# Optimization experiments

Measured on AMD Instinct MI355X. Metric: run time of the kernel, lower is better.

The kernel has to match this reference:

```python
import jax, jax.numpy as jnp
import numpy as np

B, C, H, W = 4, 128, 96, 96
E = 4
C8 = C // 8


def _conv1x1(w, b, x):
    # w: [out, in], x: [b, in, H, W]
    return jnp.einsum('oi,bihw->bohw', w, x) + b[None, :, None, None]


def _bilinear_zeros(x, gx, gy):
    # x: [b, C, h, w]; gx, gy: [b, H2, W2] normalized coords in [-1, 1]
    # align_corners=True, padding_mode='zeros' (matches F.grid_sample)
    b, c, h, w = x.shape
    ix = (gx + 1.0) * 0.5 * (w - 1)
    iy = (gy + 1.0) * 0.5 * (h - 1)
    ix0 = jnp.floor(ix)
    iy0 = jnp.floor(iy)
    tx = ix - ix0
    ty = iy - iy0
    ix0 = ix0.astype(jnp.int32)
    iy0 = iy0.astype(jnp.int32)

    def gather(yy, xx):
        valid = ((xx >= 0) & (xx < w) & (yy >= 0) & (yy < h)).astype(x.dtype)
        xc = jnp.clip(xx, 0, w - 1)
        yc = jnp.clip(yy, 0, h - 1)
        vals = jax.vmap(lambda xb, y, xi: xb[:, y, xi])(x, yc, xc)  # [b,C,H2,W2]
        return vals * valid[:, None]

    w00 = ((1 - tx) * (1 - ty))[:, None]
    w01 = (tx * (1 - ty))[:, None]
    w10 = ((1 - tx) * ty)[:, None]
    w11 = (tx * ty)[:, None]
    return (gather(iy0, ix0) * w00 + gather(iy0, ix0 + 1) * w01
            + gather(iy0 + 1, ix0) * w10 + gather(iy0 + 1, ix0 + 1) * w11)


def setup_inputs() -> dict:
    key = jax.random.key(0)
    ks = jax.random.split(key, 12)
    s = 0.05
    return {
        'x': jax.random.normal(ks[0], (B, C, H, W), jnp.float32),
        'weight_compress': jax.random.normal(ks[1], (E, C8, C), jnp.float32) * s,
        'weight_expand': jax.random.normal(ks[2], (E, C, C8), jnp.float32) * s,
        'body_w1': jax.random.normal(ks[3], (64, 3), jnp.float32) * s,
        'body_b1': jax.random.normal(ks[4], (64,), jnp.float32) * s,
        'body_w2': jax.random.normal(ks[5], (64, 64), jnp.float32) * s,
        'body_b2': jax.random.normal(ks[6], (64,), jnp.float32) * s,
        'rout_w': jax.random.normal(ks[7], (E, 64), jnp.float32) * s,
        'rout_b': jax.random.normal(ks[8], (E,), jnp.float32) * s,
        'off_w': jax.random.normal(ks[9], (2, 64), jnp.float32) * s,
        'off_b': jax.random.normal(ks[10], (2,), jnp.float32) * s,
        'scale': 2,
    }


def reference(x, weight_compress, weight_expand, body_w1, body_b1,
              body_w2, body_b2, rout_w, rout_b, off_w, off_b, scale):
    b, c, h, w = x.shape
    sc = float(scale)
    H2 = round(h * sc)
    W2 = round(w * sc)

    # fractional sub-pixel coordinates (meta-upsample positional encoding)
    ch = (jnp.arange(H2, dtype=jnp.float32) + 0.5) / sc
    ch = ch - jnp.floor(ch + 0.001) - 0.5  # [H2]
    cw = (jnp.arange(W2, dtype=jnp.float32) + 0.5) / sc
    cw = cw - jnp.floor(cw + 0.001) - 0.5  # [W2]
    inp = jnp.stack([
        jnp.full((H2, W2), 1.0 / sc, jnp.float32),
        jnp.broadcast_to(ch[:, None], (H2, W2)),
        jnp.broadcast_to(cw[None, :], (H2, W2)),
    ], axis=0)[None]  # [1, 3, H2, W2]

    emb = jax.nn.relu(_conv1x1(body_w1, body_b1, inp))
    emb = jax.nn.relu(_conv1x1(body_w2, body_b2, emb))
    offset = _conv1x1(off_w, off_b, emb)                      # [1, 2, H2, W2]
    routing = jax.nn.sigmoid(_conv1x1(rout_w, rout_b, emb))   # [1, E, H2, W2]
    r = routing[0].transpose(1, 2, 0)                         # [H2, W2, E]

    # base sampling grid, align_corners=True normalization + learned offset
    gx = ((jnp.arange(W2, dtype=jnp.float32) + 0.5) / sc - 0.5) * 2.0 / (w - 1) - 1.0
    gy = ((jnp.arange(H2, dtype=jnp.float32) + 0.5) / sc - 0.5) * 2.0 / (h - 1) - 1.0
    gx = gx[None, None, :] + offset[:, 0] * 2.0 / (w - 1)     # [1, H2, W2]
    gy = gy[None, :, None] + offset[:, 1] * 2.0 / (h - 1)
    gx = jnp.broadcast_to(gx, (b, H2, W2))
    gy = jnp.broadcast_to(gy, (b, H2, W2))

    fea0 = _bilinear_zeros(x, gx, gy)          # [b, C, H2, W2]
    fea = fea0.transpose(0, 2, 3, 1)           # [b, H2, W2, C]

    # per-pixel routed 1x1 convs: compress (C->C/8) then expand (C/8->C)
    comp = jnp.einsum('bhwc,hwe,eoc->bhwo', fea, r, weight_compress)
    out = jnp.einsum('bhwo,hwe,eco->bhwc', comp, r, weight_expand)
    return out.transpose(0, 3, 1, 2) + fea0
```

## Files before the change

### kernel.cpp

```cpp
#include <hip/hip_runtime.h>
#include <math.h>

#define Bn 4
#define Cc 128
#define Hh 96
#define Ww 96
#define H2c 192
#define W2c 192
#define HW (Hh*Ww)
#define HW2 (H2c*W2c)

#define WC_OFF 0
#define WE_OFF (4*2048)
#define TAP_OFF (8*2048)
#define M_OFF  16640

typedef float  f32x4  __attribute__((ext_vector_type(4)));
typedef short  s16x8  __attribute__((ext_vector_type(8)));

__device__ __forceinline__ unsigned f2bf(float f) {
    unsigned u = __float_as_uint(f);
    return (u + 0x7FFFu + ((u >> 16) & 1u)) >> 16;
}

__device__ __forceinline__ void gload_lds16(const float* g, float* l) {
    __builtin_amdgcn_global_load_lds(
        (const __attribute__((address_space(1))) unsigned int*)g,
        (__attribute__((address_space(3))) unsigned int*)l,
        16, 0, 0);
}

__global__ __launch_bounds__(256) void k1_mix(
    const float* __restrict__ wcomp, const float* __restrict__ wexp,
    const float* __restrict__ bw1, const float* __restrict__ bb1,
    const float* __restrict__ bw2, const float* __restrict__ bb2,
    const float* __restrict__ rw,  const float* __restrict__ rb,
    const float* __restrict__ ow,  const float* __restrict__ ob,
    float* __restrict__ ws)
{
    __shared__ float e1[64], e2[64], rr[4], of[2];
    const int tid   = threadIdx.x;
    const int cls   = blockIdx.x >> 4;
    const int chunk = blockIdx.x & 15;
    const float chv = (cls & 2) ? 0.25f : -0.25f;
    const float cwv = (cls & 1) ? 0.25f : -0.25f;

    if (tid < 64) {
        float h = bw1[tid*3+0]*0.5f + bw1[tid*3+1]*chv + bw1[tid*3+2]*cwv + bb1[tid];
        e1[tid] = fmaxf(h, 0.f);
    }
    __syncthreads();
    if (tid < 64) {
        float s = bb2[tid];
        for (int i = 0; i < 64; ++i) s += bw2[tid*64+i]*e1[i];
        e2[tid] = fmaxf(s, 0.f);
    }
    __syncthreads();
    if (tid < 6) {
        if (tid < 4) {
            float s = rb[tid];
            for (int i = 0; i < 64; ++i) s += rw[tid*64+i]*e2[i];
            rr[tid] = 1.f/(1.f+expf(-s));
        } else {
            const int d = tid - 4;
            float s = ob[d];
            for (int i = 0; i < 64; ++i) s += ow[d*64+i]*e2[i];
            of[d] = s;
        }
    }
    __syncthreads();
    const float r0 = rr[0], r1 = rr[1], r2 = rr[2], r3 = rr[3];

    if (tid < 128) {
        const int idx = chunk*128 + tid;
        const int o = idx >> 7, c = idx & 127;
        const float v = r0*wcomp[idx] + r1*wcomp[2048+idx]
                      + r2*wcomp[4096+idx] + r3*wcomp[6144+idx];
        ws[WC_OFF + cls*2048 + c*16 + o] = v;
    } else {
        const int idx = chunk*128 + (tid - 128);
        ws[WE_OFF + cls*2048 + idx] =
            r0*wexp[idx] + r1*wexp[2048+idx] + r2*wexp[4096+idx] + r3*wexp[6144+idx];
    }
    if (chunk == 0 && tid == 0) {
        const float fx = cwv + of[0];
        const float fy = chv + of[1];
        const float Dx = floorf(fx), Dy = floorf(fy);
        ws[TAP_OFF + cls*4 + 0] = fx - Dx;
        ws[TAP_OFF + cls*4 + 1] = fy - Dy;
        ws[TAP_OFF + cls*4 + 2] = Dx;
        ws[TAP_OFF + cls*4 + 3] = Dy;
    }
}

__global__ __launch_bounds__(256) void k1b_fold(
    const float* __restrict__ wsr, unsigned short* __restrict__ Mw)
{
    const int t   = blockIdx.x*256 + threadIdx.x;
    const int cls = t >> 12;
    const int rem = t & 4095;
    const int co  = rem >> 5;
    const int ci0 = (rem & 31) * 4;
    const float* we = wsr + WE_OFF + cls*2048 + co*16;

    float m[4];
    #pragma unroll
    for (int q = 0; q < 4; ++q) {
        const float* wc = wsr + WC_OFF + cls*2048 + (ci0+q)*16;
        float s = 0.f;
        #pragma unroll
        for (int o = 0; o < 16; ++o) s += we[o]*wc[o];
        if (co == ci0 + q) s += 1.f;
        m[q] = s;
    }
    uint2 v;
    v.x = f2bf(m[0]) | (f2bf(m[1]) << 16);
    v.y = f2bf(m[2]) | (f2bf(m[3]) << 16);
    *reinterpret_cast<uint2*>(Mw + (size_t)cls*16384 + co*128 + ci0) = v;
}

__device__ __forceinline__ void remap_axis(int c0, int last, float w0, float w1,
                                           int& base, float& a0, float& a1)
{
    base = min(max(c0, 0), last - 1);
    if (c0 >= 0 && c0 < last) { a0 = w0;  a1 = w1;  }
    else if (c0 == -1)        { a0 = w1;  a1 = 0.f; }
    else if (c0 == last)      { a0 = 0.f; a1 = w0;  }
    else                      { a0 = 0.f; a1 = 0.f; }
}

__global__ __launch_bounds__(256) void k2_mfma(
    const float* __restrict__ x, const float* __restrict__ wsr,
    const unsigned short* __restrict__ Mw, float* __restrict__ out)
{
    __shared__ __align__(16) unsigned short lF[64*128];
    __shared__ __align__(16) float lWin[4*2*512];

    const int tid = threadIdx.x;
    const int xl  = tid & 63;
    const int grp = tid >> 6;

    const int n = blockIdx.x;
    const int w = (n & 7)*288 + (n >> 3);
    const int cls  = w & 3;
    const int px_  = cls & 1, py = (cls >> 1) & 1;
    const int rest = w >> 2;
    const int tile = rest % 144;
    const int b    = rest / 144;
    const int jt = tile/3, xs = tile - jt*3;
    const int j0 = jt*2, i0 = xs*32;

    const unsigned short* Mc = Mw + (size_t)cls*16384;
    const int lo = xl & 15, hi = xl >> 4;
    s16x8 a[2][4];
    #pragma unroll
    for (int t = 0; t < 2; ++t)
        #pragma unroll
        for (int kk = 0; kk < 4; ++kk)
            a[t][kk] = *reinterpret_cast<const s16x8*>(
                Mc + (32*grp + 16*t + lo)*128 + kk*32 + hi*8);

    const int pr = xl >> 5, pc = xl & 31;
    const int j = j0 + pr, i = i0 + pc;

    const float tx = wsr[TAP_OFF + cls*4 + 0];
    const float ty = wsr[TAP_OFF + cls*4 + 1];
    const int   Dx = (int)wsr[TAP_OFF + cls*4 + 2];
    const int   Dy = (int)wsr[TAP_OFF + cls*4 + 3];
    int basex, basey; float ax0, ax1, ay0, ay1;
    remap_axis(i + Dx, Ww - 1, 1.f - tx, tx, basex, ax0, ax1);
    remap_axis(j + Dy, Hh - 1, 1.f - ty, ty, basey, ay0, ay1);
    const float w00 = ay0*ax0, w01 = ay0*ax1, w10 = ay1*ax0, w11 = ay1*ax1;

    const int c0  = i0 + Dx;
    const int cs0 = min(max(0, c0 & ~3), Ww - 40);
    const int cidx = basex - cs0;
    const int ro0 = pr*40 + cidx;
    const int ro1 = ro0 + 40;

    const int jD = j0 + Dy;
    const int sl = xl & 31;
    const int s2 = min(sl, 29);
    const int lr = s2 / 10, lq = s2 - lr*10;
    const int lrow = min(max(jD + lr, 0), Hh - 1);
    const float* gsrc = x + (size_t)b*Cc*HW + (size_t)lrow*Ww + cs0 + 4*lq;
    const int chsub = xl >> 5;

    float* winw = lWin + grp*1024;

#define ISSUE(q) { \
    _Pragma("unroll") \
    for (int p = 0; p < 2; ++p) \
        gload_lds16(gsrc + (size_t)(grp*32 + (q)*4 + p*2 + chsub)*HW, \
                    winw + ((q)&1)*512 + p*256); }

    ISSUE(0)
    ISSUE(1)
    #pragma unroll
    for (int q = 0; q < 8; ++q) {
        if (q < 7) asm volatile("s_waitcnt vmcnt(2)" ::: "memory");
        else       asm volatile("s_waitcnt vmcnt(0)" ::: "memory");
        __builtin_amdgcn_sched_barrier(0);
        {
            const float* wb = winw + (q&1)*512;
            float f[4];
            #pragma unroll
            for (int u = 0; u < 4; ++u) {
                const float* wc = wb + (u>>1)*256 + (u&1)*128;
                f[u] = w00*wc[ro0] + w01*wc[ro0+1] + w10*wc[ro1] + w11*wc[ro1+1];
            }
            uint2 v;
            v.x = f2bf(f[0]) | (f2bf(f[1]) << 16);
            v.y = f2bf(f[2]) | (f2bf(f[3]) << 16);
            const int c = grp*32 + q*4;
            int byte = xl*256 + c*2;
            byte ^= (xl & 7) << 4;
            *reinterpret_cast<uint2*>(reinterpret_cast<char*>(lF) + byte) = v;
        }
        if (q < 6) {
            asm volatile("s_waitcnt lgkmcnt(0)" ::: "memory");
            __builtin_amdgcn_sched_barrier(0);
            ISSUE(q+2)
        }
    }
#undef ISSUE
    __syncthreads();

    f32x4 acc[2][4];
    #pragma unroll
    for (int t = 0; t < 2; ++t)
        #pragma unroll
        for (int nn = 0; nn < 4; ++nn) acc[t][nn] = (f32x4){0.f, 0.f, 0.f, 0.f};

    #pragma unroll
    for (int kk = 0; kk < 4; ++kk) {
        #pragma unroll
        for (int nn = 0; nn < 4; ++nn) {
            int byte = (nn*16 + lo)*256 + kk*64 + hi*16;
            byte ^= (lo & 7) << 4;
            const s16x8 bf = *reinterpret_cast<const s16x8*>(
                reinterpret_cast<const char*>(lF) + byte);
            acc[0][nn] = __builtin_amdgcn_mfma_f32_16x16x32_bf16(a[0][kk], bf, acc[0][nn], 0, 0, 0);
            acc[1][nn] = __builtin_amdgcn_mfma_f32_16x16x32_bf16(a[1][kk], bf, acc[1][nn], 0, 0, 0);
        }
    }

    #pragma unroll
    for (int t = 0; t < 2; ++t)
        #pragma unroll
        for (int nn = 0; nn < 4; ++nn) {
            const int slot2 = nn*16 + lo;
            const int pr2 = slot2 >> 5, pc2 = slot2 & 31;
            const int yg = 2*(j0 + pr2) + py;
            const int xg = 2*(i0 + pc2) + px_;
            const int ch0 = 32*grp + 16*t + hi*4;
            float* op = out + ((size_t)(b*Cc + ch0)*H2c + yg)*W2c + xg;
            #pragma unroll
            for (int r = 0; r < 4; ++r)
                op[(size_t)r*HW2] = acc[t][nn][r];
        }
}

extern "C" void kernel_launch(void* const* d_in, const int* in_sizes, int n_in,
                              void* d_out, int out_size, void* d_ws, size_t ws_size,
                              hipStream_t stream) {
    const float* x     = (const float*)d_in[0];
    const float* wcomp = (const float*)d_in[1];
    const float* wexp  = (const float*)d_in[2];
    const float* bw1   = (const float*)d_in[3];
    const float* bb1   = (const float*)d_in[4];
    const float* bw2   = (const float*)d_in[5];
    const float* bb2   = (const float*)d_in[6];
    const float* rw    = (const float*)d_in[7];
    const float* rb    = (const float*)d_in[8];
    const float* ow    = (const float*)d_in[9];
    const float* ob    = (const float*)d_in[10];
    float* out = (float*)d_out;
    float* ws  = (float*)d_ws;
    unsigned short* Mw = (unsigned short*)(ws + M_OFF);

    k1_mix<<<64, 256, 0, stream>>>(wcomp, wexp, bw1, bb1, bw2, bb2, rw, rb, ow, ob, ws);
    k1b_fold<<<64, 256, 0, stream>>>(ws, Mw);
    k2_mfma<<<2304, 256, 0, stream>>>(x, ws, Mw, out);
}
```

Baseline: 45.60 us.

## Tile by output row with both x-phases per block for vectorized stores

After: 51.98 us. 1.14x slower.

```diff
diff --git a/kernel.cpp b/kernel.cpp
--- a/kernel.cpp
+++ b/kernel.cpp
@@ -140,53 +140,50 @@
     const int xl  = tid & 63;
     const int grp = tid >> 6;
 
-    const int n = blockIdx.x;
-    const int w = (n & 7)*288 + (n >> 3);
-    const int cls  = w & 3;
-    const int px_  = cls & 1, py = (cls >> 1) & 1;
-    const int rest = w >> 2;
-    const int tile = rest % 144;
-    const int b    = rest / 144;
-    const int jt = tile/3, xs = tile - jt*3;
-    const int j0 = jt*2, i0 = xs*32;
-
-    const unsigned short* Mc = Mw + (size_t)cls*16384;
-    const int lo = xl & 15, hi = xl >> 4;
-    s16x8 a[2][4];
-    #pragma unroll
-    for (int t = 0; t < 2; ++t)
-        #pragma unroll
-        for (int kk = 0; kk < 4; ++kk)
-            a[t][kk] = *reinterpret_cast<const s16x8*>(
-                Mc + (32*grp + 16*t + lo)*128 + kk*32 + hi*8);
-
-    const int pr = xl >> 5, pc = xl & 31;
-    const int j = j0 + pr, i = i0 + pc;
-
-    const float tx = wsr[TAP_OFF + cls*4 + 0];
-    const float ty = wsr[TAP_OFF + cls*4 + 1];
-    const int   Dx = (int)wsr[TAP_OFF + cls*4 + 2];
-    const int   Dy = (int)wsr[TAP_OFF + cls*4 + 3];
+    const int n  = blockIdx.x;
+    const int w  = (n & 7)*288 + (n >> 3);
+    const int b  = w / 576;
+    const int rr = w % 576;
+    const int yg = rr / 3;
+    const int xt = rr % 3;
+    const int ygp = yg & 1;
+    const int j   = yg >> 1;
+    const int i0  = xt*32;
+    const int clsE = ygp << 1;
+
+    const int px = xl & 1;
+    const int i  = i0 + (xl >> 1);
+    const int cls = clsE | px;
+
+    const float txE = wsr[TAP_OFF + clsE*4 + 0], txO = wsr[TAP_OFF + (clsE|1)*4 + 0];
+    const float tyE = wsr[TAP_OFF + clsE*4 + 1], tyO = wsr[TAP_OFF + (clsE|1)*4 + 1];
+    const int   DxE = (int)wsr[TAP_OFF + clsE*4 + 2], DxO = (int)wsr[TAP_OFF + (clsE|1)*4 + 2];
+    const int   DyE = (int)wsr[TAP_OFF + clsE*4 + 3], DyO = (int)wsr[TAP_OFF + (clsE|1)*4 + 3];
+    const float tx = px ? txO : txE;
+    const float ty = px ? tyO : tyE;
+    const int   Dx = px ? DxO : DxE;
+    const int   Dy = px ? DyO : DyE;
+
     int basex, basey; float ax0, ax1, ay0, ay1;
     remap_axis(i + Dx, Ww - 1, 1.f - tx, tx, basex, ax0, ax1);
     remap_axis(j + Dy, Hh - 1, 1.f - ty, ty, basey, ay0, ay1);
     const float w00 = ay0*ax0, w01 = ay0*ax1, w10 = ay1*ax0, w11 = ay1*ax1;
 
-    const int c0  = i0 + Dx;
-    const int cs0 = min(max(0, c0 & ~3), Ww - 40);
-    const int cidx = basex - cs0;
-    const int ro0 = pr*40 + cidx;
+    const int minDx = min(DxE, DxO), minDy = min(DyE, DyO);
+    const int cs0 = min(max((i0 + minDx) & ~3, 0), Ww - 40);
+    const int jDc = min(j + minDy, Hh - 2);
+    const int ro0 = (basey - jDc)*40 + (basex - cs0);
     const int ro1 = ro0 + 40;
 
-    const int jD = j0 + Dy;
     const int sl = xl & 31;
     const int s2 = min(sl, 29);
     const int lr = s2 / 10, lq = s2 - lr*10;
-    const int lrow = min(max(jD + lr, 0), Hh - 1);
+    const int lrow = min(max(jDc + lr, 0), Hh - 1);
     const float* gsrc = x + (size_t)b*Cc*HW + (size_t)lrow*Ww + cs0 + 4*lq;
     const int chsub = xl >> 5;
 
     float* winw = lWin + grp*1024;
+    const int slot = px*32 + (xl >> 1);
 
 #define ISSUE(q) { \
     _Pragma("unroll") \
@@ -213,8 +210,8 @@
             v.x = f2bf(f[0]) | (f2bf(f[1]) << 16);
             v.y = f2bf(f[2]) | (f2bf(f[3]) << 16);
             const int c = grp*32 + q*4;
-            int byte = xl*256 + c*2;
-            byte ^= (xl & 7) << 4;
+            int byte = slot*256 + c*2;
+            byte ^= (slot & 7) << 4;
             *reinterpret_cast<uint2*>(reinterpret_cast<char*>(lF) + byte) = v;
         }
         if (q < 6) {
@@ -226,6 +223,7 @@
 #undef ISSUE
     __syncthreads();
 
+    const int lo = xl & 15, hi = xl >> 4;
     f32x4 acc[2][4];
     #pragma unroll
     for (int t = 0; t < 2; ++t)
@@ -233,32 +231,45 @@
         for (int nn = 0; nn < 4; ++nn) acc[t][nn] = (f32x4){0.f, 0.f, 0.f, 0.f};
 
     #pragma unroll
-    for (int kk = 0; kk < 4; ++kk) {
-        #pragma unroll
-        for (int nn = 0; nn < 4; ++nn) {
-            int byte = (nn*16 + lo)*256 + kk*64 + hi*16;
-            byte ^= (lo & 7) << 4;
-            const s16x8 bf = *reinterpret_cast<const s16x8*>(
-                reinterpret_cast<const char*>(lF) + byte);
-            acc[0][nn] = __builtin_amdgcn_mfma_f32_16x16x32_bf16(a[0][kk], bf, acc[0][nn], 0, 0, 0);
-            acc[1][nn] = __builtin_amdgcn_mfma_f32_16x16x32_bf16(a[1][kk], bf, acc[1][nn], 0, 0, 0);
-        }
-    }
-
-    #pragma unroll
-    for (int t = 0; t < 2; ++t)
-        #pragma unroll
-        for (int nn = 0; nn < 4; ++nn) {
-            const int slot2 = nn*16 + lo;
-            const int pr2 = slot2 >> 5, pc2 = slot2 & 31;
-            const int yg = 2*(j0 + pr2) + py;
-            const int xg = 2*(i0 + pc2) + px_;
-            const int ch0 = 32*grp + 16*t + hi*4;
-            float* op = out + ((size_t)(b*Cc + ch0)*H2c + yg)*W2c + xg;
+    for (int ph = 0; ph < 2; ++ph) {
+        const unsigned short* Mc = Mw + (size_t)(clsE | ph)*16384;
+        s16x8 mf[2][4];
+        #pragma unroll
+        for (int t = 0; t < 2; ++t)
             #pragma unroll
-            for (int r = 0; r < 4; ++r)
-                op[(size_t)r*HW2] = acc[t][nn][r];
-        }
+            for (int kk = 0; kk < 4; ++kk)
+                mf[t][kk] = *reinterpret_cast<const s16x8*>(
+                    Mc + (32*grp + 16*t + lo)*128 + kk*32 + hi*8);
+        #pragma unroll
+        for (int kk = 0; kk < 4; ++kk) {
+            #pragma unroll
+            for (int q2 = 0; q2 < 2; ++q2) {
+                const int nn = ph*2 + q2;
+                const int row = nn*16 + lo;
+                int byte = row*256 + kk*64 + hi*16;
+                byte ^= (row & 7) << 4;
+                const s16x8 af = *reinterpret_cast<const s16x8*>(
+                    reinterpret_cast<const char*>(lF) + byte);
+                acc[0][nn] = __builtin_amdgcn_mfma_f32_16x16x32_bf16(af, mf[0][kk], acc[0][nn], 0, 0, 0);
+                acc[1][nn] = __builtin_amdgcn_mfma_f32_16x16x32_bf16(af, mf[1][kk], acc[1][nn], 0, 0, 0);
+            }
+        }
+    }
+
+    #pragma unroll
+    for (int t = 0; t < 2; ++t) {
+        const int ch = 32*grp + 16*t + lo;
+        float* rowp = out + ((size_t)(b*Cc + ch)*H2c + yg)*W2c;
+        #pragma unroll
+        for (int p = 0; p < 2; ++p) {
+            const f32x4 e = acc[t][p], o = acc[t][p+2];
+            const f32x4 v0 = {e[0], o[0], e[1], o[1]};
+            const f32x4 v1 = {e[2], o[2], e[3], o[3]};
+            float* op = rowp + 2*i0 + p*32 + hi*8;
+            *reinterpret_cast<f32x4*>(op)     = v0;
+            *reinterpret_cast<f32x4*>(op + 4) = v1;
+        }
+    }
 }
 
 extern "C" void kernel_launch(void* const* d_in, const int* in_sizes, int n_in,
```

## Fuse weight mixing into fold kernel and process two row tiles per block

Applied to the files above, without the earlier changes.

Measured after the change: 55.36 us. 1.21x slower.

```diff
diff --git a/kernel.cpp b/kernel.cpp
--- a/kernel.cpp
+++ b/kernel.cpp
@@ -10,10 +10,8 @@
 #define HW (Hh*Ww)
 #define HW2 (H2c*W2c)
 
-#define WC_OFF 0
-#define WE_OFF (4*2048)
-#define TAP_OFF (8*2048)
-#define M_OFF  16640
+#define TAP_OFF 0
+#define M_OFF 16
 
 typedef float  f32x4  __attribute__((ext_vector_type(4)));
 typedef short  s16x8  __attribute__((ext_vector_type(8)));
@@ -26,19 +24,18 @@
 __device__ __forceinline__ void gload_lds16(const float* g, float* l) {
     __builtin_amdgcn_global_load_lds(
         (const __attribute__((address_space(1))) unsigned int*)g,
-        (__attribute__((address_space(3))) unsigned int*)l,
-        16, 0, 0);
-}
-
-__global__ __launch_bounds__(256) void k1_mix(
+        (__attribute__((address_space(3))) unsigned int*)l, 16, 0, 0);
+}
+
+__global__ __launch_bounds__(256) void k1_prep(
     const float* __restrict__ wcomp, const float* __restrict__ wexp,
     const float* __restrict__ bw1, const float* __restrict__ bb1,
     const float* __restrict__ bw2, const float* __restrict__ bb2,
     const float* __restrict__ rw,  const float* __restrict__ rb,
     const float* __restrict__ ow,  const float* __restrict__ ob,
-    float* __restrict__ ws)
+    float* __restrict__ ws, unsigned short* __restrict__ Mw)
 {
-    __shared__ float e1[64], e2[64], rr[4], of[2];
+    __shared__ float e1[64], e2[64], rr4[4], of2[2];
     const int tid   = threadIdx.x;
     const int cls   = blockIdx.x >> 4;
     const int chunk = blockIdx.x & 15;
@@ -60,57 +57,47 @@
         if (tid < 4) {
             float s = rb[tid];
             for (int i = 0; i < 64; ++i) s += rw[tid*64+i]*e2[i];
-            rr[tid] = 1.f/(1.f+expf(-s));
+            rr4[tid] = 1.f/(1.f+expf(-s));
         } else {
             const int d = tid - 4;
             float s = ob[d];
             for (int i = 0; i < 64; ++i) s += ow[d*64+i]*e2[i];
-            of[d] = s;
+            of2[d] = s;
         }
     }
     __syncthreads();
-    const float r0 = rr[0], r1 = rr[1], r2 = rr[2], r3 = rr[3];
-
-    if (tid < 128) {
-        const int idx = chunk*128 + tid;
-        const int o = idx >> 7, c = idx & 127;
-        const float v = r0*wcomp[idx] + r1*wcomp[2048+idx]
-                      + r2*wcomp[4096+idx] + r3*wcomp[6144+idx];
-        ws[WC_OFF + cls*2048 + c*16 + o] = v;
-    } else {
-        const int idx = chunk*128 + (tid - 128);
-        ws[WE_OFF + cls*2048 + idx] =
-            r0*wexp[idx] + r1*wexp[2048+idx] + r2*wexp[4096+idx] + r3*wexp[6144+idx];
-    }
+    const float r0 = rr4[0], r1 = rr4[1], r2 = rr4[2], r3 = rr4[3];
+
     if (chunk == 0 && tid == 0) {
-        const float fx = cwv + of[0];
-        const float fy = chv + of[1];
+        const float fx = cwv + of2[0];
+        const float fy = chv + of2[1];
         const float Dx = floorf(fx), Dy = floorf(fy);
         ws[TAP_OFF + cls*4 + 0] = fx - Dx;
         ws[TAP_OFF + cls*4 + 1] = fy - Dy;
         ws[TAP_OFF + cls*4 + 2] = Dx;
         ws[TAP_OFF + cls*4 + 3] = Dy;
     }
-}
-
-__global__ __launch_bounds__(256) void k1b_fold(
-    const float* __restrict__ wsr, unsigned short* __restrict__ Mw)
-{
-    const int t   = blockIdx.x*256 + threadIdx.x;
-    const int cls = t >> 12;
-    const int rem = t & 4095;
-    const int co  = rem >> 5;
-    const int ci0 = (rem & 31) * 4;
-    const float* we = wsr + WE_OFF + cls*2048 + co*16;
-
+
+    const int co  = chunk*8 + (tid >> 5);
+    const int ci0 = (tid & 31) * 4;
+    const float* weB = wexp + co*16;
+    float wem[16];
+    #pragma unroll
+    for (int o = 0; o < 16; ++o)
+        wem[o] = r0*weB[o] + r1*weB[2048+o] + r2*weB[4096+o] + r3*weB[6144+o];
     float m[4];
     #pragma unroll
     for (int q = 0; q < 4; ++q) {
-        const float* wc = wsr + WC_OFF + cls*2048 + (ci0+q)*16;
+        const int ci = ci0 + q;
+        const float* wcB = wcomp + ci;
         float s = 0.f;
         #pragma unroll
-        for (int o = 0; o < 16; ++o) s += we[o]*wc[o];
-        if (co == ci0 + q) s += 1.f;
+        for (int o = 0; o < 16; ++o) {
+            const float wcm = r0*wcB[o*128]        + r1*wcB[2048 + o*128]
+                            + r2*wcB[4096 + o*128] + r3*wcB[6144 + o*128];
+            s += wem[o]*wcm;
+        }
+        if (co == ci) s += 1.f;
         m[q] = s;
     }
     uint2 v;
@@ -141,14 +128,15 @@
     const int grp = tid >> 6;
 
     const int n = blockIdx.x;
-    const int w = (n & 7)*288 + (n >> 3);
+    const int w = (n & 7)*144 + (n >> 3);
     const int cls  = w & 3;
     const int px_  = cls & 1, py = (cls >> 1) & 1;
     const int rest = w >> 2;
-    const int tile = rest % 144;
-    const int b    = rest / 144;
-    const int jt = tile/3, xs = tile - jt*3;
-    const int j0 = jt*2, i0 = xs*32;
+    const int b    = rest / 72;
+    const int pr72 = rest % 72;
+    const int jt = pr72 / 3, xs = pr72 % 3;
+    const int j0A = jt*4, j0B = jt*4 + 2;
+    const int i0  = xs*32;
 
     const unsigned short* Mc = Mw + (size_t)cls*16384;
     const int lo = xl & 15, hi = xl >> 4;
@@ -161,104 +149,116 @@
                 Mc + (32*grp + 16*t + lo)*128 + kk*32 + hi*8);
 
     const int pr = xl >> 5, pc = xl & 31;
-    const int j = j0 + pr, i = i0 + pc;
-
+    const int i  = i0 + pc;
     const float tx = wsr[TAP_OFF + cls*4 + 0];
     const float ty = wsr[TAP_OFF + cls*4 + 1];
     const int   Dx = (int)wsr[TAP_OFF + cls*4 + 2];
     const int   Dy = (int)wsr[TAP_OFF + cls*4 + 3];
-    int basex, basey; float ax0, ax1, ay0, ay1;
+
+    int basex; float ax0, ax1;
     remap_axis(i + Dx, Ww - 1, 1.f - tx, tx, basex, ax0, ax1);
-    remap_axis(j + Dy, Hh - 1, 1.f - ty, ty, basey, ay0, ay1);
-    const float w00 = ay0*ax0, w01 = ay0*ax1, w10 = ay1*ax0, w11 = ay1*ax1;
-
-    const int c0  = i0 + Dx;
-    const int cs0 = min(max(0, c0 & ~3), Ww - 40);
+    int baseyA, baseyB; float ay0A, ay1A, ay0B, ay1B;
+    remap_axis(j0A + pr + Dy, Hh - 1, 1.f - ty, ty, baseyA, ay0A, ay1A);
+    remap_axis(j0B + pr + Dy, Hh - 1, 1.f - ty, ty, baseyB, ay0B, ay1B);
+    const float w00A = ay0A*ax0, w01A = ay0A*ax1, w10A = ay1A*ax0, w11A = ay1A*ax1;
+    const float w00B = ay0B*ax0, w01B = ay0B*ax1, w10B = ay1B*ax0, w11B = ay1B*ax1;
+
+    const int cs0  = min(max((i0 + Dx) & ~3, 0), Ww - 40);
     const int cidx = basex - cs0;
-    const int ro0 = pr*40 + cidx;
-    const int ro1 = ro0 + 40;
-
-    const int jD = j0 + Dy;
-    const int sl = xl & 31;
-    const int s2 = min(sl, 29);
+    const int ro0  = pr*40 + cidx, ro1 = ro0 + 40;
+
+    const int sl = xl & 31, s2 = min(sl, 29);
     const int lr = s2 / 10, lq = s2 - lr*10;
-    const int lrow = min(max(jD + lr, 0), Hh - 1);
-    const float* gsrc = x + (size_t)b*Cc*HW + (size_t)lrow*Ww + cs0 + 4*lq;
     const int chsub = xl >> 5;
+    const int lrowA = min(max(j0A + Dy + lr, 0), Hh - 1);
+    const int lrowB = min(max(j0B + Dy + lr, 0), Hh - 1);
+    const float* gsrcA = x + (size_t)b*Cc*HW + (size_t)lrowA*Ww + cs0 + 4*lq;
+    const float* gsrcB = x + (size_t)b*Cc*HW + (size_t)lrowB*Ww + cs0 + 4*lq;
 
     float* winw = lWin + grp*1024;
 
-#define ISSUE(q) { \
+#define ISSUE(gs, q) { \
     _Pragma("unroll") \
     for (int p = 0; p < 2; ++p) \
-        gload_lds16(gsrc + (size_t)(grp*32 + (q)*4 + p*2 + chsub)*HW, \
+        gload_lds16((gs) + (size_t)(grp*32 + (q)*4 + p*2 + chsub)*HW, \
                     winw + ((q)&1)*512 + p*256); }
 
-    ISSUE(0)
-    ISSUE(1)
-    #pragma unroll
-    for (int q = 0; q < 8; ++q) {
-        if (q < 7) asm volatile("s_waitcnt vmcnt(2)" ::: "memory");
-        else       asm volatile("s_waitcnt vmcnt(0)" ::: "memory");
-        __builtin_amdgcn_sched_barrier(0);
-        {
-            const float* wb = winw + (q&1)*512;
-            float f[4];
-            #pragma unroll
-            for (int u = 0; u < 4; ++u) {
-                const float* wc = wb + (u>>1)*256 + (u&1)*128;
-                f[u] = w00*wc[ro0] + w01*wc[ro0+1] + w10*wc[ro1] + w11*wc[ro1+1];
-            }
-            uint2 v;
-            v.x = f2bf(f[0]) | (f2bf(f[1]) << 16);
-            v.y = f2bf(f[2]) | (f2bf(f[3]) << 16);
-            const int c = grp*32 + q*4;
-            int byte = xl*256 + c*2;
-            byte ^= (xl & 7) << 4;
-            *reinterpret_cast<uint2*>(reinterpret_cast<char*>(lF) + byte) = v;
-        }
-        if (q < 6) {
-            asm volatile("s_waitcnt lgkmcnt(0)" ::: "memory");
-            __builtin_amdgcn_sched_barrier(0);
-            ISSUE(q+2)
-        }
-    }
+#define PRODUCE(gs, W00, W01, W10, W11) { \
+    ISSUE(gs, 0) \
+    ISSUE(gs, 1) \
+    _Pragma("unroll") \
+    for (int q = 0; q < 8; ++q) { \
+        if (q < 7) asm volatile("s_waitcnt vmcnt(2)" ::: "memory"); \
+        else       asm volatile("s_waitcnt vmcnt(0)" ::: "memory"); \
+        __builtin_amdgcn_sched_barrier(0); \
+        { \
+            const float* wb = winw + (q&1)*512; \
+            float f[4]; \
+            _Pragma("unroll") \
+            for (int u = 0; u < 4; ++u) { \
+                const float* wc = wb + (u>>1)*256 + (u&1)*128; \
+                f[u] = (W00)*wc[ro0] + (W01)*wc[ro0+1] + (W10)*wc[ro1] + (W11)*wc[ro1+1]; \
+            } \
+            uint2 v; \
+            v.x = f2bf(f[0]) | (f2bf(f[1]) << 16); \
+            v.y = f2bf(f[2]) | (f2bf(f[3]) << 16); \
+            const int c = grp*32 + q*4; \
+            int byte = xl*256 + c*2; \
+            byte ^= (xl & 7) << 4; \
+            *reinterpret_cast<uint2*>(reinterpret_cast<char*>(lF) + byte) = v; \
+        } \
+        if (q < 6) { \
+            asm volatile("s_waitcnt lgkmcnt(0)" ::: "memory"); \
+            __builtin_amdgcn_sched_barrier(0); \
+            ISSUE(gs, q+2) \
+        } \
+    } }
+
+#define GEMM_STORE(J0) { \
+    f32x4 acc[2][4]; \
+    _Pragma("unroll") \
+    for (int t = 0; t < 2; ++t) \
+        _Pragma("unroll") \
+        for (int nn = 0; nn < 4; ++nn) acc[t][nn] = (f32x4){0.f, 0.f, 0.f, 0.f}; \
+    _Pragma("unroll") \
+    for (int kk = 0; kk < 4; ++kk) { \
+        _Pragma("unroll") \
+        for (int nn = 0; nn < 4; ++nn) { \
+            int byte = (nn*16 + lo)*256 + kk*64 + hi*16; \
+            byte ^= (lo & 7) << 4; \
+            const s16x8 bf = *reinterpret_cast<const s16x8*>( \
+                reinterpret_cast<const char*>(lF) + byte); \
+            acc[0][nn] = __builtin_amdgcn_mfma_f32_16x16x32_bf16(a[0][kk], bf, acc[0][nn], 0, 0, 0); \
+            acc[1][nn] = __builtin_amdgcn_mfma_f32_16x16x32_bf16(a[1][kk], bf, acc[1][nn], 0, 0, 0); \
+        } \
+    } \
+    _Pragma("unroll") \
+    for (int t = 0; t < 2; ++t) \
+        _Pragma("unroll") \
+        for (int nn = 0; nn < 4; ++nn) { \
+            const int slot2 = nn*16 + lo; \
+            const int pr2 = slot2 >> 5, pc2 = slot2 & 31; \
+            const int yg = 2*((J0) + pr2) + py; \
+            const int xg = 2*(i0 + pc2) + px_; \
+            const int ch0 = 32*grp + 16*t + hi*4; \
+            float* op = out + ((size_t)(b*Cc + ch0)*H2c + yg)*W2c + xg; \
+            _Pragma("unroll") \
+            for (int r = 0; r < 4; ++r) \
+                op[(size_t)r*HW2] = acc[t][nn][r]; \
+        } }
+
+    PRODUCE(gsrcA, w00A, w01A, w10A, w11A)
+    __syncthreads();
+    GEMM_STORE(j0A)
+    __syncthreads();
+
+    PRODUCE(gsrcB, w00B, w01B, w10B, w11B)
+    __syncthreads();
+    GEMM_STORE(j0B)
+
 #undef ISSUE
-    __syncthreads();
-
-    f32x4 acc[2][4];
-    #pragma unroll
-    for (int t = 0; t < 2; ++t)
-        #pragma unroll
-        for (int nn = 0; nn < 4; ++nn) acc[t][nn] = (f32x4){0.f, 0.f, 0.f, 0.f};
-
-    #pragma unroll
-    for (int kk = 0; kk < 4; ++kk) {
-        #pragma unroll
-        for (int nn = 0; nn < 4; ++nn) {
-            int byte = (nn*16 + lo)*256 + kk*64 + hi*16;
-            byte ^= (lo & 7) << 4;
-            const s16x8 bf = *reinterpret_cast<const s16x8*>(
-                reinterpret_cast<const char*>(lF) + byte);
-            acc[0][nn] = __builtin_amdgcn_mfma_f32_16x16x32_bf16(a[0][kk], bf, acc[0][nn], 0, 0, 0);
-            acc[1][nn] = __builtin_amdgcn_mfma_f32_16x16x32_bf16(a[1][kk], bf, acc[1][nn], 0, 0, 0);
-        }
-    }
-
-    #pragma unroll
-    for (int t = 0; t < 2; ++t)
-        #pragma unroll
-        for (int nn = 0; nn < 4; ++nn) {
-            const int slot2 = nn*16 + lo;
-            const int pr2 = slot2 >> 5, pc2 = slot2 & 31;
-            const int yg = 2*(j0 + pr2) + py;
-            const int xg = 2*(i0 + pc2) + px_;
-            const int ch0 = 32*grp + 16*t + hi*4;
-            float* op = out + ((size_t)(b*Cc + ch0)*H2c + yg)*W2c + xg;
-            #pragma unroll
-            for (int r = 0; r < 4; ++r)
-                op[(size_t)r*HW2] = acc[t][nn][r];
-        }
+#undef PRODUCE
+#undef GEMM_STORE
 }
 
 extern "C" void kernel_launch(void* const* d_in, const int* in_sizes, int n_in,
@@ -279,7 +279,7 @@
     float* ws  = (float*)d_ws;
     unsigned short* Mw = (unsigned short*)(ws + M_OFF);
 
-    k1_mix<<<64, 256, 0, stream>>>(wcomp, wexp, bw1, bb1, bw2, bb2, rw, rb, ow, ob, ws);
-    k1b_fold<<<64, 256, 0, stream>>>(ws, Mw);
-    k2_mfma<<<2304, 256, 0, stream>>>(x, ws, Mw, out);
-}
+    k1_prep<<<64, 256, 0, stream>>>(wcomp, wexp, bw1, bb1, bw2, bb2,
+                                    rw, rb, ow, ob, ws, Mw);
+    k2_mfma<<<1152, 256, 0, stream>>>(x, ws, Mw, out);
+}
```

## Fuse weight mixing into fold kernel and pack two tiles per 512-thread block

Applied to the files above, without the earlier changes.

After: 58.52 us. +28.3%, slower.

```diff
diff --git a/kernel.cpp b/kernel.cpp
--- a/kernel.cpp
+++ b/kernel.cpp
@@ -10,10 +10,8 @@
 #define HW (Hh*Ww)
 #define HW2 (H2c*W2c)
 
-#define WC_OFF 0
-#define WE_OFF (4*2048)
-#define TAP_OFF (8*2048)
-#define M_OFF  16640
+#define TAP_OFF 0
+#define M_OFF 16
 
 typedef float  f32x4  __attribute__((ext_vector_type(4)));
 typedef short  s16x8  __attribute__((ext_vector_type(8)));
@@ -26,19 +24,18 @@
 __device__ __forceinline__ void gload_lds16(const float* g, float* l) {
     __builtin_amdgcn_global_load_lds(
         (const __attribute__((address_space(1))) unsigned int*)g,
-        (__attribute__((address_space(3))) unsigned int*)l,
-        16, 0, 0);
-}
-
-__global__ __launch_bounds__(256) void k1_mix(
+        (__attribute__((address_space(3))) unsigned int*)l, 16, 0, 0);
+}
+
+__global__ __launch_bounds__(256) void k1_prep(
     const float* __restrict__ wcomp, const float* __restrict__ wexp,
     const float* __restrict__ bw1, const float* __restrict__ bb1,
     const float* __restrict__ bw2, const float* __restrict__ bb2,
     const float* __restrict__ rw,  const float* __restrict__ rb,
     const float* __restrict__ ow,  const float* __restrict__ ob,
-    float* __restrict__ ws)
+    float* __restrict__ ws, unsigned short* __restrict__ Mw)
 {
-    __shared__ float e1[64], e2[64], rr[4], of[2];
+    __shared__ float e1[64], e2[64], rr4[4], of2[2];
     const int tid   = threadIdx.x;
     const int cls   = blockIdx.x >> 4;
     const int chunk = blockIdx.x & 15;
@@ -60,57 +57,47 @@
         if (tid < 4) {
             float s = rb[tid];
             for (int i = 0; i < 64; ++i) s += rw[tid*64+i]*e2[i];
-            rr[tid] = 1.f/(1.f+expf(-s));
+            rr4[tid] = 1.f/(1.f+expf(-s));
         } else {
             const int d = tid - 4;
             float s = ob[d];
             for (int i = 0; i < 64; ++i) s += ow[d*64+i]*e2[i];
-            of[d] = s;
-        }
-    }
-    __syncthreads();
-    const float r0 = rr[0], r1 = rr[1], r2 = rr[2], r3 = rr[3];
-
-    if (tid < 128) {
-        const int idx = chunk*128 + tid;
-        const int o = idx >> 7, c = idx & 127;
-        const float v = r0*wcomp[idx] + r1*wcomp[2048+idx]
-                      + r2*wcomp[4096+idx] + r3*wcomp[6144+idx];
-        ws[WC_OFF + cls*2048 + c*16 + o] = v;
-    } else {
-        const int idx = chunk*128 + (tid - 128);
-        ws[WE_OFF + cls*2048 + idx] =
-            r0*wexp[idx] + r1*wexp[2048+idx] + r2*wexp[4096+idx] + r3*wexp[6144+idx];
-    }
+            of2[d] = s;
+        }
+    }
+    __syncthreads();
+    const float r0 = rr4[0], r1 = rr4[1], r2 = rr4[2], r3 = rr4[3];
+
     if (chunk == 0 && tid == 0) {
-        const float fx = cwv + of[0];
-        const float fy = chv + of[1];
+        const float fx = cwv + of2[0];
+        const float fy = chv + of2[1];
         const float Dx = floorf(fx), Dy = floorf(fy);
         ws[TAP_OFF + cls*4 + 0] = fx - Dx;
         ws[TAP_OFF + cls*4 + 1] = fy - Dy;
         ws[TAP_OFF + cls*4 + 2] = Dx;
         ws[TAP_OFF + cls*4 + 3] = Dy;
     }
-}
-
-__global__ __launch_bounds__(256) void k1b_fold(
-    const float* __restrict__ wsr, unsigned short* __restrict__ Mw)
-{
-    const int t   = blockIdx.x*256 + threadIdx.x;
-    const int cls = t >> 12;
-    const int rem = t & 4095;
-    const int co  = rem >> 5;
-    const int ci0 = (rem & 31) * 4;
-    const float* we = wsr + WE_OFF + cls*2048 + co*16;
-
+
+    const int co  = chunk*8 + (tid >> 5);
+    const int ci0 = (tid & 31) * 4;
+    const float* weB = wexp + co*16;
+    float wem[16];
+    #pragma unroll
+    for (int o = 0; o < 16; ++o)
+        wem[o] = r0*weB[o] + r1*weB[2048+o] + r2*weB[4096+o] + r3*weB[6144+o];
     float m[4];
     #pragma unroll
     for (int q = 0; q < 4; ++q) {
-        const float* wc = wsr + WC_OFF + cls*2048 + (ci0+q)*16;
+        const int ci = ci0 + q;
+        const float* wcB = wcomp + ci;
         float s = 0.f;
         #pragma unroll
-        for (int o = 0; o < 16; ++o) s += we[o]*wc[o];
-        if (co == ci0 + q) s += 1.f;
+        for (int o = 0; o < 16; ++o) {
+            const float wcm = r0*wcB[o*128]        + r1*wcB[2048 + o*128]
+                            + r2*wcB[4096 + o*128] + r3*wcB[6144 + o*128];
+            s += wem[o]*wcm;
+        }
+        if (co == ci) s += 1.f;
         m[q] = s;
     }
     uint2 v;
@@ -129,19 +116,21 @@
     else                      { a0 = 0.f; a1 = 0.f; }
 }
 
-__global__ __launch_bounds__(256) void k2_mfma(
+__global__ __launch_bounds__(512, 4) void k2_mfma(
     const float* __restrict__ x, const float* __restrict__ wsr,
     const unsigned short* __restrict__ Mw, float* __restrict__ out)
 {
-    __shared__ __align__(16) unsigned short lF[64*128];
-    __shared__ __align__(16) float lWin[4*2*512];
+    __shared__ __align__(16) unsigned short lF[2*64*128];
+    __shared__ __align__(16) float lWin[8*1024];
 
     const int tid = threadIdx.x;
     const int xl  = tid & 63;
-    const int grp = tid >> 6;
-
-    const int n = blockIdx.x;
-    const int w = (n & 7)*288 + (n >> 3);
+    const int grp = (tid >> 6) & 3;
+    const int sg  = tid >> 8;
+
+    const int n    = blockIdx.x;
+    const int base = (n & 7)*144 + (n >> 3);
+    const int w    = base*2 + sg;
     const int cls  = w & 3;
     const int px_  = cls & 1, py = (cls >> 1) & 1;
     const int rest = w >> 2;
@@ -149,6 +138,8 @@
     const int b    = rest / 144;
     const int jt = tile/3, xs = tile - jt*3;
     const int j0 = jt*2, i0 = xs*32;
+
+    unsigned short* lFs = lF + sg*8192;
 
     const unsigned short* Mc = Mw + (size_t)cls*16384;
     const int lo = xl & 15, hi = xl >> 4;
@@ -186,7 +177,7 @@
     const float* gsrc = x + (size_t)b*Cc*HW + (size_t)lrow*Ww + cs0 + 4*lq;
     const int chsub = xl >> 5;
 
-    float* winw = lWin + grp*1024;
+    float* winw = lWin + (tid >> 6)*1024;
 
 #define ISSUE(q) { \
     _Pragma("unroll") \
@@ -215,7 +206,7 @@
             const int c = grp*32 + q*4;
             int byte = xl*256 + c*2;
             byte ^= (xl & 7) << 4;
-            *reinterpret_cast<uint2*>(reinterpret_cast<char*>(lF) + byte) = v;
+            *reinterpret_cast<uint2*>(reinterpret_cast<char*>(lFs) + byte) = v;
         }
         if (q < 6) {
             asm volatile("s_waitcnt lgkmcnt(0)" ::: "memory");
@@ -239,7 +230,7 @@
             int byte = (nn*16 + lo)*256 + kk*64 + hi*16;
             byte ^= (lo & 7) << 4;
             const s16x8 bf = *reinterpret_cast<const s16x8*>(
-                reinterpret_cast<const char*>(lF) + byte);
+                reinterpret_cast<const char*>(lFs) + byte);
             acc[0][nn] = __builtin_amdgcn_mfma_f32_16x16x32_bf16(a[0][kk], bf, acc[0][nn], 0, 0, 0);
             acc[1][nn] = __builtin_amdgcn_mfma_f32_16x16x32_bf16(a[1][kk], bf, acc[1][nn], 0, 0, 0);
         }
@@ -279,7 +270,7 @@
     float* ws  = (float*)d_ws;
     unsigned short* Mw = (unsigned short*)(ws + M_OFF);
 
-    k1_mix<<<64, 256, 0, stream>>>(wcomp, wexp, bw1, bb1, bw2, bb2, rw, rb, ow, ob, ws);
-    k1b_fold<<<64, 256, 0, stream>>>(ws, Mw);
-    k2_mfma<<<2304, 256, 0, stream>>>(x, ws, Mw, out);
-}
+    k1_prep<<<64, 256, 0, stream>>>(wcomp, wexp, bw1, bb1, bw2, bb2,
+                                    rw, rb, ow, ob, ws, Mw);
+    k2_mfma<<<1152, 512, 0, stream>>>(x, ws, Mw, out);
+}
```
